# Performance work log

Hardware: AMD Instinct MI355X
Metric: run time of the kernel (lower is better)

Reference implementation:

```python
import jax, jax.numpy as jnp
import numpy as np

B, L, HID, NH, HD = 2, 2048, 1024, 16, 64


def _positions_and_segs(lengths):
    # lengths: (L,) int64, sub-sequence lengths packed at front, zeros pad.
    cs = jnp.cumsum(lengths)                       # (L,) segment end offsets
    t = jnp.arange(lengths.shape[0])
    seg = jnp.searchsorted(cs, t, side='right')    # segment id per token
    seg = jnp.minimum(seg, lengths.shape[0] - 1)
    starts = cs - lengths                          # segment start offsets
    pos = t - starts[seg]                          # position reset per segment
    valid = t < cs[-1]
    return jnp.where(valid, pos, 0), seg, valid


def _rope(x, positions):
    # x: (B, L, H, D); positions: (B, L)
    d = x.shape[-1]
    inv_freq = 1.0 / (10000.0 ** (jnp.arange(0, d, 2, dtype=jnp.float32) / d))
    freqs = positions[..., None].astype(jnp.float32) * inv_freq   # (B, L, d/2)
    emb = jnp.concatenate([freqs, freqs], axis=-1)                # (B, L, d)
    cos = jnp.cos(emb)[:, :, None, :]
    sin = jnp.sin(emb)[:, :, None, :]
    x1, x2 = jnp.split(x, 2, axis=-1)
    rot = jnp.concatenate([-x2, x1], axis=-1)
    return x * cos + rot * sin


def setup_inputs() -> dict:
    key = jax.random.key(0)
    ks = jax.random.split(key, 5)
    hidden_states = jax.random.normal(ks[0], (B, L, HID), dtype=jnp.float32)
    aml = np.zeros((B, L), dtype=np.int64)
    aml[0, :3] = [512, 768, 520]    # sums to 1800 (248 padding tokens)
    aml[1, :3] = [1024, 512, 512]   # sums to 2048 (no padding)
    attention_mask_in_length = jnp.asarray(aml)
    Wqkv = jax.random.normal(ks[1], (HID, 3 * HID), dtype=jnp.float32) * 0.02
    bqkv = jax.random.normal(ks[2], (3 * HID,), dtype=jnp.float32) * 0.02
    Wout = jax.random.normal(ks[3], (HID, HID), dtype=jnp.float32) * 0.02
    bout = jax.random.normal(ks[4], (HID,), dtype=jnp.float32) * 0.02
    return {"hidden_states": hidden_states,
            "attention_mask_in_length": attention_mask_in_length,
            "Wqkv": Wqkv, "bqkv": bqkv, "Wout": Wout, "bout": bout}


def reference(hidden_states, attention_mask_in_length, Wqkv, bqkv, Wout, bout):
    Bb, Ll, _ = hidden_states.shape
    qkv = hidden_states @ Wqkv + bqkv                 # (B, L, 3*HID)
    qkv = qkv.reshape(Bb, Ll, 3, NH, HD)
    q, k, v = qkv[:, :, 0], qkv[:, :, 1], qkv[:, :, 2]
    scale = HD ** -0.5
    q = q * scale  # module pre-scales q before RoPE
    positions, seg, valid = jax.vmap(_positions_and_segs)(attention_mask_in_length)
    q = _rope(q, positions)
    k = _rope(k, positions)
    # block-diagonal attention: only within same sub-sequence, valid tokens
    mask = (seg[:, :, None] == seg[:, None, :]) & valid[:, :, None] & valid[:, None, :]
    # flash_attn with softmax_scale=None applies head_dim**-0.5 again (faithful)
    scores = jnp.einsum('bihd,bjhd->bhij', q, k) * scale
    scores = jnp.where(mask[:, None, :, :], scores, -1e9)
    probs = jax.nn.softmax(scores, axis=-1)
    out = jnp.einsum('bhij,bjhd->bihd', probs, v)     # (B, L, H, D)
    out = jnp.where(valid[:, :, None, None], out, 0.0)  # pad_input zeros padding rows
    out = out.reshape(Bb, Ll, NH * HD)
    return out @ Wout + bout
```

## Files before the change

### kernel.cpp

```cpp
#include <hip/hip_runtime.h>
#include <math.h>

#define B_ 2
#define L_ 2048
#define HID_ 1024
#define NH_ 16
#define HD_ 64
#define QBLK 128

typedef unsigned short u16;
typedef __attribute__((ext_vector_type(8))) _Float16 half8;
typedef __attribute__((ext_vector_type(4))) float f32x4;

__device__ __forceinline__ u16 f2h(float x) {
    _Float16 h = (_Float16)x; u16 r; __builtin_memcpy(&r, &h, 2); return r;
}
__device__ __forceinline__ float fexp2(float x) {
    float r;
    asm("v_exp_f32 %0, %1" : "=v"(r) : "v"(x));
    return r;
}
__device__ __forceinline__ unsigned pkrtz(float a, float b) {
    auto v = __builtin_amdgcn_cvt_pkrtz(a, b);
    unsigned r; __builtin_memcpy(&r, &v, 4); return r;
}
__device__ __forceinline__ void gload16(const void* g, void* l) {
    __builtin_amdgcn_global_load_lds(
        (const __attribute__((address_space(1))) void*)g,
        (__attribute__((address_space(3))) void*)l, 16, 0, 0);
}

__global__ void setup_kernel(const int* __restrict__ aml,
                             int* __restrict__ sstart, int* __restrict__ send,
                             int* __restrict__ poss_out)
{
    const int b = blockIdx.x;
    const int tid = threadIdx.x;
    __shared__ int cs[L_];
    __shared__ int partial[256];

    int vals[8];
    const int t0 = tid * 8;
    int s = 0;
#pragma unroll
    for (int e = 0; e < 8; ++e) { vals[e] = aml[b * L_ + t0 + e]; s += vals[e]; }
    partial[tid] = s;
    __syncthreads();
    if (tid == 0) {
        int acc = 0;
        for (int i = 0; i < 256; ++i) { int tmp = partial[i]; partial[i] = acc; acc += tmp; }
    }
    __syncthreads();
    int off = partial[tid];
#pragma unroll
    for (int e = 0; e < 8; ++e) { off += vals[e]; cs[t0 + e] = off; }
    __syncthreads();

    const int total = cs[L_ - 1];
    for (int t = tid; t < L_; t += 256) {
        int lo = 0, hi = L_;
        while (lo < hi) { int mid = (lo + hi) >> 1; if (cs[mid] <= t) lo = mid + 1; else hi = mid; }
        int seg = lo < (L_ - 1) ? lo : (L_ - 1);
        int end = cs[seg];
        int len = aml[b * L_ + seg];
        int start = end - len;
        bool valid = t < total;
        poss_out[b * L_ + t] = valid ? (t - start) : 0;
        sstart[b * L_ + t] = valid ? start : 0x7fffffff;
        send[b * L_ + t]   = valid ? end : 0;
    }
}

__global__ void trig_kernel(const int* __restrict__ poss,
                            float* __restrict__ ctab, float* __restrict__ stab)
{
    const double kexp = 13.287712379549449 / 32.0;
    int idx = blockIdx.x * 256 + threadIdx.x;
    int d = idx & 31;
    int bt = idx >> 5;
    double f = (double)poss[bt] * exp2(-(double)d * kexp);
    ctab[idx] = (float)cos(f);
    stab[idx] = (float)sin(f);
}

__global__ void conv_all(const float* __restrict__ hidden, u16* __restrict__ hidh,
                         const float* __restrict__ Wqkv, u16* __restrict__ wqh,
                         const float* __restrict__ Wout, u16* __restrict__ woh)
{
    __shared__ float t[32][33];
    const int bid = blockIdx.x;
    const int tid = threadIdx.x;
    if (bid < 4096) {
        int i = (bid * 256 + tid) * 4;
        float4 v = *(const float4*)&hidden[i];
        *(ushort4*)&hidh[i] = make_ushort4(f2h(v.x), f2h(v.y), f2h(v.z), f2h(v.w));
        return;
    }
    const float* W; u16* o; int Kd = 1024, Nd, n0, k0;
    if (bid < 7168) {
        int idx = bid - 4096; W = Wqkv; o = wqh; Nd = 3072;
        n0 = (idx % 96) * 32; k0 = (idx / 96) * 32;
    } else {
        int idx = bid - 7168; W = Wout; o = woh; Nd = 1024;
        n0 = (idx & 31) * 32; k0 = (idx >> 5) * 32;
    }
    const int r = tid >> 5, c = tid & 31;
#pragma unroll
    for (int i = 0; i < 4; ++i)
        t[r + 8 * i][c] = W[(size_t)(k0 + r + 8 * i) * Nd + n0 + c];
    __syncthreads();
#pragma unroll
    for (int i = 0; i < 4; ++i)
        o[(size_t)(n0 + r + 8 * i) * Kd + k0 + c] = f2h(t[c][r + 8 * i]);
}

template <int MODE>
__global__ __launch_bounds__(256, 3)
void gemm_mfma(const u16* __restrict__ Ap, const u16* __restrict__ Bp,
               const float* __restrict__ bias, float* __restrict__ C,
               u16* __restrict__ qb, u16* __restrict__ kb, u16* __restrict__ vtb,
               const float* __restrict__ ctab, const float* __restrict__ stab,
               int M, int N, int K)
{
    __shared__ u16 Asl[128 * 64];
    __shared__ u16 Bsl[128 * 64];

    const int tid = threadIdx.x;
    const int wave = tid >> 6, lane = tid & 63;

    const int nwg = gridDim.x * gridDim.y;
    const int bid = blockIdx.y * gridDim.x + blockIdx.x;
    const int cpx = nwg >> 3;
    const int swz = (bid & 7) * cpx + (bid >> 3);
    const int brow = (swz / gridDim.x) * 128;
    const int bcol = (swz % gridDim.x) * 128;

    const int wr = (wave >> 1) * 64, wc = (wave & 1) * 64;
    const int grow = tid >> 3, gslot = tid & 7;
    const int fr = lane & 15, kg = lane >> 4;

    f32x4 acc[4][4];
#pragma unroll
    for (int m = 0; m < 4; ++m)
#pragma unroll
        for (int n = 0; n < 4; ++n) acc[m][n] = (f32x4){0.f, 0.f, 0.f, 0.f};

    for (int ka = 0; ka < K; ka += 64) {
#pragma unroll
        for (int c = 0; c < 4; ++c) {
            int row = c * 32 + grow;
            int sg = gslot ^ (row & 7);
            gload16(&Ap[(size_t)(brow + row) * K + ka + sg * 8],
                    (char*)Asl + c * 4096 + wave * 1024);
            gload16(&Bp[(size_t)(bcol + row) * K + ka + sg * 8],
                    (char*)Bsl + c * 4096 + wave * 1024);
        }
        __syncthreads();

#pragma unroll
        for (int kk = 0; kk < 2; ++kk) {
            half8 af[4], bfv[4];
            const int cbase = kk * 4 + kg;
#pragma unroll
            for (int n = 0; n < 4; ++n) {
                int r = wc + n * 16 + fr;
                bfv[n] = *(const half8*)&Bsl[r * 64 + ((cbase ^ (r & 7)) << 3)];
            }
#pragma unroll
            for (int m = 0; m < 4; ++m) {
                int r = wr + m * 16 + fr;
                af[m] = *(const half8*)&Asl[r * 64 + ((cbase ^ (r & 7)) << 3)];
            }
#pragma unroll
            for (int m = 0; m < 4; ++m)
#pragma unroll
                for (int n = 0; n < 4; ++n)
                    acc[m][n] = __builtin_amdgcn_mfma_f32_16x16x32_f16(
                        af[m], bfv[n], acc[m][n], 0, 0, 0);
        }
        __syncthreads();
    }

    const int cr = (lane >> 4) * 4;
    const int cc = lane & 15;
    if (MODE == 0) {
#pragma unroll
        for (int m = 0; m < 4; ++m) {
#pragma unroll
            for (int n = 0; n < 4; ++n) {
                const int col = bcol + wc + n * 16 + cc;
                const float bv = bias[col];
                const int row0 = brow + wr + m * 16 + cr;
#pragma unroll
                for (int rg = 0; rg < 4; ++rg)
                    C[(size_t)(row0 + rg) * N + col] = acc[m][n][rg] + bv;
            }
        }
    } else {
        const int colbase = bcol + wc;
        const int sel = colbase >> 10;
        const int hh = (colbase & 1023) >> 6;
#pragma unroll
        for (int m = 0; m < 4; ++m) {
            const int row0 = brow + wr + m * 16 + cr;
            const int bidx = row0 >> 11, t0 = row0 & (L_ - 1);
            if (sel == 2) {
#pragma unroll
                for (int n = 0; n < 4; ++n) {
                    int col = colbase + n * 16 + cc;
                    float bv = bias[col];
                    int d = col & 63;
                    ushort4 pk = make_ushort4(
                        f2h(acc[m][n][0] + bv), f2h(acc[m][n][1] + bv),
                        f2h(acc[m][n][2] + bv), f2h(acc[m][n][3] + bv));
                    *(ushort4*)&vtb[((((size_t)bidx * NH_ + hh) * HD_) + d) * L_ + t0] = pk;
                }
            } else {
                u16* dst = (sel == 0) ? qb : kb;
#pragma unroll
                for (int np = 0; np < 2; ++np) {
                    int col1 = colbase + np * 16 + cc;
                    int d1 = np * 16 + cc;
                    float bv1 = bias[col1], bv2 = bias[col1 + 32];
#pragma unroll
                    for (int rg = 0; rg < 4; ++rg) {
                        int t = t0 + rg;
                        float c = ctab[((size_t)bidx * L_ + t) * 32 + d1];
                        float s = stab[((size_t)bidx * L_ + t) * 32 + d1];
                        float x1 = acc[m][np][rg] + bv1;
                        float x2 = acc[m][np + 2][rg] + bv2;
                        size_t base = ((((size_t)bidx * NH_ + hh) * L_) + t) * (size_t)HD_;
                        dst[base + d1]      = f2h(x1 * c - x2 * s);
                        dst[base + d1 + 32] = f2h(x2 * c + x1 * s);
                    }
                }
            }
        }
    }
}

__global__ __launch_bounds__(512)
void attn_mfma(const u16* __restrict__ qb, const u16* __restrict__ kbuf,
               const u16* __restrict__ vt, const int* __restrict__ sstart,
               const int* __restrict__ send, u16* __restrict__ ohi)
{
    __shared__ u16 Ksb[2][64 * 64];
    __shared__ u16 Vsb[2][64 * 64];
    __shared__ u16 Pw[8][16 * 64];
    __shared__ int ss[QBLK], se[QBLK];

    const int b = blockIdx.z, h = blockIdx.y, q0 = blockIdx.x * QBLK;
    const int tid = threadIdx.x, wave = tid >> 6, lane = tid & 63;
    const int fr = lane & 15, kg = lane >> 4;
    const size_t hb = (((size_t)b * NH_) + h) * (size_t)(L_ * HD_);
    const size_t hv = (((size_t)b * NH_) + h) * (size_t)(HD_ * L_);

    if (tid < QBLK) { ss[tid] = sstart[b * L_ + q0 + tid]; se[tid] = send[b * L_ + q0 + tid]; }

    const u16* qrow = &qb[hb + (size_t)(q0 + wave * 16 + fr) * HD_ + kg * 8];
    half8 qf0 = *(const half8*)(qrow);
    half8 qf1 = *(const half8*)(qrow + 32);
    __syncthreads();

    int kmin = 0x7fffffff, kmax = 0;
#pragma unroll 8
    for (int r = 0; r < QBLK; ++r) { kmin = min(kmin, ss[r]); kmax = max(kmax, se[r]); }

    const int myss_ = ss[wave * 16 + fr];
    const int myse_ = se[wave * 16 + fr];

    float l_ = 0.f;
    f32x4 oacc[4];
#pragma unroll
    for (int i = 0; i < 4; ++i) oacc[i] = (f32x4){0.f, 0.f, 0.f, 0.f};

    const int grow = tid >> 3;
    const int sg = (tid & 7) ^ (grow & 7);
    const float SCL = 0.015625f * 1.4426950408889634f;
    const int fx = fr & 7;
    u16* pwl = &Pw[wave][fr * 64];

    const int kt_first = kmin & ~63;
    if (kt_first < kmax) {
        gload16(&kbuf[hb + (size_t)(kt_first + grow) * HD_ + sg * 8],
                (char*)Ksb[0] + wave * 1024);
        gload16(&vt[hv + (size_t)grow * L_ + kt_first + sg * 8],
                (char*)Vsb[0] + wave * 1024);
    }
    __syncthreads();

    int bufi = 0;
    for (int kt0 = kt_first; kt0 < kmax; kt0 += 64) {
        if (kt0 + 64 < kmax) {
            gload16(&kbuf[hb + (size_t)(kt0 + 64 + grow) * HD_ + sg * 8],
                    (char*)Ksb[bufi ^ 1] + wave * 1024);
            gload16(&vt[hv + (size_t)grow * L_ + kt0 + 64 + sg * 8],
                    (char*)Vsb[bufi ^ 1] + wave * 1024);
        }
        const u16* Ks = Ksb[bufi];
        const u16* Vs = Vsb[bufi];

        f32x4 sc4[4];
#pragma unroll
        for (int ct = 0; ct < 4; ++ct) sc4[ct] = (f32x4){0.f, 0.f, 0.f, 0.f};
        __builtin_amdgcn_s_setprio(1);
#pragma unroll
        for (int kk = 0; kk < 2; ++kk) {
            half8 qf = kk ? qf1 : qf0;
#pragma unroll
            for (int ct = 0; ct < 4; ++ct) {
                int r = ct * 16 + fr;
                half8 kf = *(const half8*)&Ks[r * 64 + (((kk * 4 + kg) ^ (r & 7)) << 3)];
                sc4[ct] = __builtin_amdgcn_mfma_f32_16x16x32_f16(kf, qf, sc4[ct], 0, 0, 0);
            }
        }
        __builtin_amdgcn_s_setprio(0);

        float p[4][4];
        float psum = 0.f;
        if (__all((kt0 >= myss_) && (kt0 + 64 <= myse_))) {
#pragma unroll
            for (int ct = 0; ct < 4; ++ct)
#pragma unroll
                for (int reg = 0; reg < 4; ++reg) {
                    float e = fexp2(sc4[ct][reg] * SCL);
                    p[ct][reg] = e;
                    psum += e;
                }
        } else {
            const int ktb = kt0 + kg * 4;
#pragma unroll
            for (int ct = 0; ct < 4; ++ct)
#pragma unroll
                for (int reg = 0; reg < 4; ++reg) {
                    int kt = ktb + ct * 16 + reg;
                    bool v = (kt >= myss_) && (kt < myse_);
                    float e = fexp2(sc4[ct][reg] * SCL);
                    p[ct][reg] = v ? e : 0.f;
                    psum += p[ct][reg];
                }
        }
        psum += __shfl_xor(psum, 16);
        psum += __shfl_xor(psum, 32);
        l_ += psum;

#pragma unroll
        for (int ct = 0; ct < 4; ++ct) {
            uint2 w;
            w.x = pkrtz(p[ct][0], p[ct][1]);
            w.y = pkrtz(p[ct][2], p[ct][3]);
            *(uint2*)&pwl[(((2 * ct + (kg >> 1)) ^ fx) << 3) + (kg & 1) * 4] = w;
        }

        __builtin_amdgcn_s_setprio(1);
#pragma unroll
        for (int ks2 = 0; ks2 < 2; ++ks2) {
            half8 pf = *(const half8*)&pwl[((4 * ks2 + kg) ^ fx) << 3];
#pragma unroll
            for (int dt = 0; dt < 4; ++dt) {
                int r = dt * 16 + fr;
                half8 vf = *(const half8*)&Vs[r * 64 + (((ks2 * 4 + kg) ^ (r & 7)) << 3)];
                oacc[dt] = __builtin_amdgcn_mfma_f32_16x16x32_f16(vf, pf, oacc[dt], 0, 0, 0);
            }
        }
        __builtin_amdgcn_s_setprio(0);
        __syncthreads();
        bufi ^= 1;
    }

    const int t = q0 + wave * 16 + fr;
    const float inv = (myss_ < myse_) ? 1.f / l_ : 0.f;
    const size_t rowbase = ((size_t)b * L_ + t) * (size_t)HID_ + h * HD_ + kg * 4;
#pragma unroll
    for (int dt = 0; dt < 4; ++dt) {
        *(ushort4*)&ohi[rowbase + dt * 16] = make_ushort4(
            f2h(oacc[dt][0] * inv), f2h(oacc[dt][1] * inv),
            f2h(oacc[dt][2] * inv), f2h(oacc[dt][3] * inv));
    }
}

extern "C" void kernel_launch(void* const* d_in, const int* in_sizes, int n_in,
                              void* d_out, int out_size, void* d_ws, size_t ws_size,
                              hipStream_t stream)
{
    (void)in_sizes; (void)n_in; (void)out_size; (void)ws_size;
    const float* hidden = (const float*)d_in[0];
    const int*   aml    = (const int*)d_in[1];
    const float* Wqkv   = (const float*)d_in[2];
    const float* bqkv   = (const float*)d_in[3];
    const float* Wout   = (const float*)d_in[4];
    const float* bout   = (const float*)d_in[5];
    float* out = (float*)d_out;

    const size_t per = (size_t)B_ * NH_ * L_ * HD_;
    float* ctab = (float*)d_ws;
    float* stab = ctab + (size_t)B_ * L_ * 32;
    int* sstart = (int*)(stab + (size_t)B_ * L_ * 32);
    int* send   = sstart + B_ * L_;
    int* poss   = send + B_ * L_;
    u16* qbf  = (u16*)(poss + B_ * L_);
    u16* kbf  = qbf + per;
    u16* vtb  = kbf + per;
    u16* hidh = vtb + per;
    u16* wqh  = hidh + (size_t)4096 * 1024;
    u16* woh  = wqh + (size_t)3072 * 1024;

    setup_kernel<<<dim3(B_), dim3(256), 0, stream>>>(aml, sstart, send, poss);
    trig_kernel<<<dim3((B_ * L_ * 32) / 256), dim3(256), 0, stream>>>(poss, ctab, stab);

    conv_all<<<dim3(8192), dim3(256), 0, stream>>>(hidden, hidh, Wqkv, wqh, Wout, woh);

    gemm_mfma<1><<<dim3(24, 32), dim3(256), 0, stream>>>(
        hidh, wqh, bqkv, nullptr, qbf, kbf, vtb, ctab, stab,
        B_ * L_, 3 * HID_, HID_);

    attn_mfma<<<dim3(L_ / QBLK, NH_, B_), dim3(512), 0, stream>>>(
        qbf, kbf, vtb, sstart, send, hidh);

    gemm_mfma<0><<<dim3(8, 32), dim3(256), 0, stream>>>(
        hidh, woh, bout, out, nullptr, nullptr, nullptr, nullptr, nullptr,
        B_ * L_, HID_, HID_);
}
```

Before: 107.3 us.

## Software-pipeline PV MFMA with next softmax and fuse trig into conversion kernel

```diff
diff --git a/kernel.cpp b/kernel.cpp
--- a/kernel.cpp
+++ b/kernel.cpp
@@ -71,21 +71,11 @@
     }
 }
 
-__global__ void trig_kernel(const int* __restrict__ poss,
-                            float* __restrict__ ctab, float* __restrict__ stab)
-{
-    const double kexp = 13.287712379549449 / 32.0;
-    int idx = blockIdx.x * 256 + threadIdx.x;
-    int d = idx & 31;
-    int bt = idx >> 5;
-    double f = (double)poss[bt] * exp2(-(double)d * kexp);
-    ctab[idx] = (float)cos(f);
-    stab[idx] = (float)sin(f);
-}
-
 __global__ void conv_all(const float* __restrict__ hidden, u16* __restrict__ hidh,
                          const float* __restrict__ Wqkv, u16* __restrict__ wqh,
-                         const float* __restrict__ Wout, u16* __restrict__ woh)
+                         const float* __restrict__ Wout, u16* __restrict__ woh,
+                         const int* __restrict__ poss,
+                         float* __restrict__ ctab, float* __restrict__ stab)
 {
     __shared__ float t[32][33];
     const int bid = blockIdx.x;
@@ -94,6 +84,16 @@
         int i = (bid * 256 + tid) * 4;
         float4 v = *(const float4*)&hidden[i];
         *(ushort4*)&hidh[i] = make_ushort4(f2h(v.x), f2h(v.y), f2h(v.z), f2h(v.w));
+        return;
+    }
+    if (bid >= 8192) {
+        const double kexp = 13.287712379549449 / 32.0;
+        int idx = (bid - 8192) * 256 + tid;
+        int d = idx & 31;
+        int bt = idx >> 5;
+        double f = (double)poss[bt] * exp2(-(double)d * kexp);
+        ctab[idx] = (float)cos(f);
+        stab[idx] = (float)sin(f);
         return;
     }
     const float* W; u16* o; int Kd = 1024, Nd, n0, k0;
@@ -245,8 +245,8 @@
                const int* __restrict__ send, u16* __restrict__ ohi)
 {
     __shared__ u16 Ksb[2][64 * 64];
-    __shared__ u16 Vsb[2][64 * 64];
-    __shared__ u16 Pw[8][16 * 64];
+    __shared__ u16 Vsb[3][64 * 64];
+    __shared__ u16 Pw[8 * 2 * 16 * 64];
     __shared__ int ss[QBLK], se[QBLK];
 
     const int b = blockIdx.z, h = blockIdx.y, q0 = blockIdx.x * QBLK;
@@ -278,10 +278,11 @@
     const int sg = (tid & 7) ^ (grow & 7);
     const float SCL = 0.015625f * 1.4426950408889634f;
     const int fx = fr & 7;
-    u16* pwl = &Pw[wave][fr * 64];
 
     const int kt_first = kmin & ~63;
-    if (kt_first < kmax) {
+    const int ntile = (kmax > kt_first) ? ((kmax - kt_first + 63) >> 6) : 0;
+
+    if (ntile > 0) {
         gload16(&kbuf[hb + (size_t)(kt_first + grow) * HD_ + sg * 8],
                 (char*)Ksb[0] + wave * 1024);
         gload16(&vt[hv + (size_t)grow * L_ + kt_first + sg * 8],
@@ -289,16 +290,9 @@
     }
     __syncthreads();
 
-    int bufi = 0;
-    for (int kt0 = kt_first; kt0 < kmax; kt0 += 64) {
-        if (kt0 + 64 < kmax) {
-            gload16(&kbuf[hb + (size_t)(kt0 + 64 + grow) * HD_ + sg * 8],
-                    (char*)Ksb[bufi ^ 1] + wave * 1024);
-            gload16(&vt[hv + (size_t)grow * L_ + kt0 + 64 + sg * 8],
-                    (char*)Vsb[bufi ^ 1] + wave * 1024);
-        }
-        const u16* Ks = Ksb[bufi];
-        const u16* Vs = Vsb[bufi];
+    for (int i = 0; i < ntile; ++i) {
+        const int kt0 = kt_first + i * 64;
+        const u16* Ks = Ksb[i & 1];
 
         f32x4 sc4[4];
 #pragma unroll
@@ -315,6 +309,31 @@
             }
         }
         __builtin_amdgcn_s_setprio(0);
+
+        if (i + 1 < ntile) {
+            const int ktn = kt0 + 64;
+            gload16(&kbuf[hb + (size_t)(ktn + grow) * HD_ + sg * 8],
+                    (char*)Ksb[(i + 1) & 1] + wave * 1024);
+            gload16(&vt[hv + (size_t)grow * L_ + ktn + sg * 8],
+                    (char*)Vsb[(i + 1) % 3] + wave * 1024);
+        }
+
+        if (i > 0) {
+            const u16* Vsp = Vsb[(i - 1) % 3];
+            const u16* pwr = &Pw[((wave << 1) + ((i - 1) & 1)) * 1024 + fr * 64];
+            __builtin_amdgcn_s_setprio(1);
+#pragma unroll
+            for (int ks2 = 0; ks2 < 2; ++ks2) {
+                half8 pf = *(const half8*)&pwr[((4 * ks2 + kg) ^ fx) << 3];
+#pragma unroll
+                for (int dt = 0; dt < 4; ++dt) {
+                    int r = dt * 16 + fr;
+                    half8 vf = *(const half8*)&Vsp[r * 64 + (((ks2 * 4 + kg) ^ (r & 7)) << 3)];
+                    oacc[dt] = __builtin_amdgcn_mfma_f32_16x16x32_f16(vf, pf, oacc[dt], 0, 0, 0);
+                }
+            }
+            __builtin_amdgcn_s_setprio(0);
+        }
 
         float p[4][4];
         float psum = 0.f;
@@ -344,28 +363,32 @@
         psum += __shfl_xor(psum, 32);
         l_ += psum;
 
+        u16* pww = &Pw[((wave << 1) + (i & 1)) * 1024 + fr * 64];
 #pragma unroll
         for (int ct = 0; ct < 4; ++ct) {
             uint2 w;
             w.x = pkrtz(p[ct][0], p[ct][1]);
             w.y = pkrtz(p[ct][2], p[ct][3]);
-            *(uint2*)&pwl[(((2 * ct + (kg >> 1)) ^ fx) << 3) + (kg & 1) * 4] = w;
-        }
-
-        __builtin_amdgcn_s_setprio(1);
+            *(uint2*)&pww[(((2 * ct + (kg >> 1)) ^ fx) << 3) + (kg & 1) * 4] = w;
+        }
+
+        __syncthreads();
+    }
+
+    if (ntile > 0) {
+        const int i = ntile;
+        const u16* Vsp = Vsb[(i - 1) % 3];
+        const u16* pwr = &Pw[((wave << 1) + ((i - 1) & 1)) * 1024 + fr * 64];
 #pragma unroll
         for (int ks2 = 0; ks2 < 2; ++ks2) {
-            half8 pf = *(const half8*)&pwl[((4 * ks2 + kg) ^ fx) << 3];
+            half8 pf = *(const half8*)&pwr[((4 * ks2 + kg) ^ fx) << 3];
 #pragma unroll
             for (int dt = 0; dt < 4; ++dt) {
                 int r = dt * 16 + fr;
-                half8 vf = *(const half8*)&Vs[r * 64 + (((ks2 * 4 + kg) ^ (r & 7)) << 3)];
+                half8 vf = *(const half8*)&Vsp[r * 64 + (((ks2 * 4 + kg) ^ (r & 7)) << 3)];
                 oacc[dt] = __builtin_amdgcn_mfma_f32_16x16x32_f16(vf, pf, oacc[dt], 0, 0, 0);
             }
         }
-        __builtin_amdgcn_s_setprio(0);
-        __syncthreads();
-        bufi ^= 1;
     }
 
     const int t = q0 + wave * 16 + fr;
@@ -406,9 +429,9 @@
     u16* woh  = wqh + (size_t)3072 * 1024;
 
     setup_kernel<<<dim3(B_), dim3(256), 0, stream>>>(aml, sstart, send, poss);
-    trig_kernel<<<dim3((B_ * L_ * 32) / 256), dim3(256), 0, stream>>>(poss, ctab, stab);
-
-    conv_all<<<dim3(8192), dim3(256), 0, stream>>>(hidden, hidh, Wqkv, wqh, Wout, woh);
+
+    conv_all<<<dim3(8704), dim3(256), 0, stream>>>(hidden, hidh, Wqkv, wqh,
+                                                   Wout, woh, poss, ctab, stab);
 
     gemm_mfma<1><<<dim3(24, 32), dim3(256), 0, stream>>>(
         hidh, wqh, bqkv, nullptr, qbf, kbf, vtb, ctab, stab,
```

Measured after the change: 108.7 us. No clear change (+1.3%).
